# Kernel tuning notes

Measured on AMD Instinct MI355X. Metric: run time of the kernel, lower is better.

The kernel has to match this reference:

```python
import jax, jax.numpy as jnp
import numpy as np

B, T, N, F_IN = 8, 288, 2000, 1
E, ID, H, K = 128, 16, 128, 20
FL = T // 2 + 1  # rfft length = in_len//2 + 1
EPS_NORM = 1e-12
EPS_LN = 1e-8


def setup_inputs() -> dict:
    key = jax.random.key(0)
    k0, k1, k2, k3, k4 = jax.random.split(key, 5)
    return {
        "x": jax.random.normal(k0, (B, T, N, F_IN), jnp.float32),
        "Ex": jax.random.normal(k1, (FL, E), jnp.float32),
        "nodes": jax.random.normal(k2, (N, ID), jnp.float32),
        "Wd": jax.random.normal(k3, (N, E + ID, H), jnp.float32),
        "Wxabs": jax.random.normal(k4, (H, H), jnp.float32),
    }


def reference(x, Ex, nodes, Wd, Wxabs):
    # [B,T,N,F] -> take feature 0 -> [B,N,T]
    xt = jnp.transpose(x[:, :, :, 0], (0, 2, 1))
    xf = jnp.abs(jnp.fft.rfft(xt, axis=-1))  # [B,N,FL]
    # F.normalize p=2 over dim=1 (nodes), then dim=2 (freq): x / max(||x||, eps)
    xf = xf / jnp.clip(jnp.sqrt(jnp.sum(xf * xf, axis=1, keepdims=True)), EPS_NORM)
    xf = xf / jnp.clip(jnp.sqrt(jnp.sum(xf * xf, axis=2, keepdims=True)), EPS_NORM)
    xe = jnp.matmul(xf, Ex)  # [B,N,E]
    # cat(): append static node identity embedding per batch element
    xk = jnp.concatenate(
        [xe, jnp.broadcast_to(nodes, (xe.shape[0], N, ID))], axis=-1
    )  # [B,N,E+ID]
    # per-node weight bmm: [N,B,E+ID] @ [N,E+ID,H] -> [B,N,H]
    x1 = jax.nn.relu(jnp.einsum('bnd,ndh->bnh', xk, Wd))
    # LayerNorm over last two dims [N,H], eps=1e-8, no affine
    mu = jnp.mean(x1, axis=(1, 2), keepdims=True)
    var = jnp.mean((x1 - mu) ** 2, axis=(1, 2), keepdims=True)
    x2 = (x1 - mu) / jnp.sqrt(var + EPS_LN)
    # dropout is identity at inference
    adp = jnp.einsum('bnh,hk->bnk', x2, Wxabs)  # convt
    adj = jnp.einsum('bnh,bmh->bnm', adp, x1)  # [B,N,N]
    adp = jax.nn.relu(adj)
    # dy_mask_graph: per-row topk over dim=2 (torch dim=1 of the [N,N] slice),
    # binary mask via scatter of ones, then elementwise mask
    _, idx = jax.lax.top_k(adp, K)  # [B,N,K]
    bi = jnp.arange(adp.shape[0])[:, None, None]
    ni = jnp.arange(N)[None, :, None]
    mask = jnp.zeros_like(adp).at[bi, ni, idx].set(1.0)
    adj_masked = adp * mask
    return jax.nn.softmax(adj_masked, axis=2)
```

## Files before the change

### kernel.cpp

```cpp
#include <hip/hip_runtime.h>
#include <math.h>

#define BB 8
#define TT 288
#define NN 2000
#define FLEN 145
#define EE 128
#define IDD 16
#define HH 128
#define DKK 144
#define KTOP 20

typedef _Float16 half8 __attribute__((ext_vector_type(8)));
typedef float f32x4 __attribute__((ext_vector_type(4)));
typedef unsigned short ushort_t;

#define OFF_TW  ((size_t)0)
#define SZ_TW   ((size_t)TT*FLEN*2)
#define OFF_XF  (OFF_TW + SZ_TW)
#define SZ_XF   ((size_t)BB*FLEN*NN)
#define OFF_ICN (OFF_XF + SZ_XF)
#define OFF_IRN (OFF_ICN + (size_t)BB*FLEN)
#define OFF_XE  (OFF_IRN + (size_t)BB*NN)
#define SZ_BNH  ((size_t)BB*NN*HH)
#define OFF_X1  (OFF_XE + SZ_BNH)
#define OFF_ADP (OFF_X1 + SZ_BNH)
#define OFF_CSW (OFF_ADP + SZ_BNH)
#define OFF_LNS (OFF_CSW + HH)
#define OFF_LNF (OFF_LNS + 16)

__device__ __forceinline__ float wredSum(float v) {
#pragma unroll
  for (int o = 32; o > 0; o >>= 1) v += __shfl_down(v, o, 64);
  return v;
}
__device__ __forceinline__ float wredMax(float v) {
#pragma unroll
  for (int o = 32; o > 0; o >>= 1) v = fmaxf(v, __shfl_down(v, o, 64));
  return v;
}
__device__ __forceinline__ float wredSumAll(float v) {
#pragma unroll
  for (int o = 32; o > 0; o >>= 1) v += __shfl_xor(v, o, 64);
  return v;
}
__device__ __forceinline__ float wredMaxAll(float v) {
#pragma unroll
  for (int o = 32; o > 0; o >>= 1) v = fmaxf(v, __shfl_xor(v, o, 64));
  return v;
}

__device__ __forceinline__ void split16(float v, ushort_t& hi, ushort_t& lo) {
  _Float16 h = (_Float16)v;
  _Float16 l = (_Float16)(v - (float)h);
  union { _Float16 f; ushort_t u; } a, b;
  a.f = h; b.f = l;
  hi = a.u; lo = b.u;
}

__global__ void k_init(const float* __restrict__ Wx, float* __restrict__ csw,
                       float* __restrict__ lns) {
  int k = threadIdx.x;
  float s = 0.f;
  for (int h = 0; h < HH; ++h) s += Wx[h * HH + k];
  csw[k] = s;
  if (k < 16) lns[k] = 0.f;
}

__global__ void k_tw(float* __restrict__ tw) {
  int id = blockIdx.x * 256 + threadIdx.x;
  if (id >= TT * FLEN) return;
  int t = id / FLEN, f = id % FLEN;
  int r = (t * f) % TT;
  double th = -2.0 * 3.14159265358979323846 * (double)r / (double)TT;
  tw[2 * id]     = (float)cos(th);
  tw[2 * id + 1] = (float)sin(th);
}

__global__ void k_dft(const float* __restrict__ x, const float* __restrict__ tw,
                      float* __restrict__ xf) {
  __shared__ __align__(16) float Xs[16][128];
  __shared__ __align__(16) float TWs[16][32][2];
  const int b = blockIdx.z;
  const int f0 = blockIdx.y * 32;
  const int n0 = blockIdx.x * 128;
  const int tid = threadIdx.x;
  const int tn = tid & 31;
  const int tf = tid >> 5;
  float ar[4][4] = {}, ai[4][4] = {};
  for (int t0 = 0; t0 < TT; t0 += 16) {
    __syncthreads();
    for (int l = tid; l < 512; l += 256) {
      int row = l >> 5, q = l & 31;
      int n = n0 + q * 4;
      const float* src = x + ((size_t)b * TT + (t0 + row)) * NN + n;
      float4 v = make_float4(0, 0, 0, 0);
      if (n + 3 < NN) v = *(const float4*)src;
      else {
        if (n + 0 < NN) v.x = src[0];
        if (n + 1 < NN) v.y = src[1];
        if (n + 2 < NN) v.z = src[2];
        if (n + 3 < NN) v.w = src[3];
      }
      *(float4*)&Xs[row][q * 4] = v;
    }
    for (int l = tid; l < 512; l += 256) {
      int row = l >> 5, ff = l & 31;
      int f = f0 + ff;
      float2 cs = make_float2(0, 0);
      if (f < FLEN) cs = *(const float2*)&tw[((size_t)(t0 + row) * FLEN + f) * 2];
      *(float2*)&TWs[row][ff][0] = cs;
    }
    __syncthreads();
#pragma unroll 4
    for (int t = 0; t < 16; ++t) {
      float4 xv = *(float4*)&Xs[t][tn * 4];
      float xx[4] = {xv.x, xv.y, xv.z, xv.w};
      float4 p0 = *(float4*)&TWs[t][tf * 4][0];
      float4 p1 = *(float4*)&TWs[t][tf * 4 + 2][0];
      float c[4] = {p0.x, p0.z, p1.x, p1.z};
      float s[4] = {p0.y, p0.w, p1.y, p1.w};
#pragma unroll
      for (int i = 0; i < 4; ++i)
#pragma unroll
        for (int j = 0; j < 4; ++j) {
          ar[i][j] = fmaf(xx[j], c[i], ar[i][j]);
          ai[i][j] = fmaf(xx[j], s[i], ai[i][j]);
        }
    }
  }
#pragma unroll
  for (int i = 0; i < 4; ++i) {
    int f = f0 + tf * 4 + i;
    if (f >= FLEN) continue;
    float* dst = &xf[((size_t)b * FLEN + f) * NN];
    float o[4];
#pragma unroll
    for (int j = 0; j < 4; ++j)
      o[j] = sqrtf(ar[i][j] * ar[i][j] + ai[i][j] * ai[i][j]);
    int n = n0 + tn * 4;
    if (n + 3 < NN) *(float4*)&dst[n] = make_float4(o[0], o[1], o[2], o[3]);
    else {
#pragma unroll
      for (int j = 0; j < 4; ++j) if (n + j < NN) dst[n + j] = o[j];
    }
  }
}

__global__ void k_colnorm(const float* __restrict__ xf, float* __restrict__ icn) {
  __shared__ float sc[4];
  int bf = blockIdx.x;
  const float* rowp = xf + (size_t)bf * NN;
  float s = 0.f;
  for (int i = threadIdx.x; i < NN; i += 256) { float v = rowp[i]; s = fmaf(v, v, s); }
  s = wredSum(s);
  int lane = threadIdx.x & 63, w = threadIdx.x >> 6;
  if (lane == 0) sc[w] = s;
  __syncthreads();
  if (threadIdx.x == 0)
    icn[bf] = 1.f / fmaxf(sqrtf(sc[0] + sc[1] + sc[2] + sc[3]), 1e-12f);
}

__global__ void k_rownorm(const float* __restrict__ xf, const float* __restrict__ icn,
                          float* __restrict__ irn) {
  int b = blockIdx.y;
  int n = blockIdx.x * 256 + threadIdx.x;
  if (n >= NN) return;
  float s = 0.f;
  for (int f = 0; f < FLEN; ++f) {
    float v = xf[((size_t)b * FLEN + f) * NN + n] * icn[b * FLEN + f];
    s = fmaf(v, v, s);
  }
  irn[b * NN + n] = 1.f / fmaxf(sqrtf(s), 1e-12f);
}

__global__ void k_xe(const float* __restrict__ xf, const float* __restrict__ icn,
                     const float* __restrict__ irn, const float* __restrict__ Ex,
                     float* __restrict__ xe) {
  __shared__ __align__(16) float As[16][64];
  __shared__ __align__(16) float Bs[16][128];
  const int b = blockIdx.y;
  const int n0 = blockIdx.x * 64;
  const int tid = threadIdx.x;
  const int tn = tid >> 4, te = tid & 15;
  float acc[4][8] = {};
  for (int f0 = 0; f0 < 160; f0 += 16) {
    __syncthreads();
    {
      int kt = tid >> 4, q = tid & 15;
      int f = f0 + kt;
      int n = n0 + q * 4;
      float4 v = make_float4(0, 0, 0, 0);
      if (f < FLEN) {
        float ic = icn[b * FLEN + f];
        const float* src = &xf[((size_t)b * FLEN + f) * NN + n];
        if (n + 3 < NN) v = *(const float4*)src;
        else {
          if (n + 0 < NN) v.x = src[0];
          if (n + 1 < NN) v.y = src[1];
          if (n + 2 < NN) v.z = src[2];
          if (n + 3 < NN) v.w = src[3];
        }
        v.x *= ic; v.y *= ic; v.z *= ic; v.w *= ic;
      }
      *(float4*)&As[kt][q * 4] = v;
    }
    for (int l = tid; l < 512; l += 256) {
      int kt = l >> 5, q = l & 31;
      int f = f0 + kt;
      float4 v = make_float4(0, 0, 0, 0);
      if (f < FLEN) v = *(const float4*)&Ex[(size_t)f * EE + q * 4];
      *(float4*)&Bs[kt][q * 4] = v;
    }
    __syncthreads();
#pragma unroll
    for (int k = 0; k < 16; ++k) {
      float4 a  = *(float4*)&As[k][tn * 4];
      float4 b0 = *(float4*)&Bs[k][te * 4];
      float4 b1 = *(float4*)&Bs[k][64 + te * 4];
      float av[4] = {a.x, a.y, a.z, a.w};
      float bv[8] = {b0.x, b0.y, b0.z, b0.w, b1.x, b1.y, b1.z, b1.w};
#pragma unroll
      for (int i = 0; i < 4; ++i)
#pragma unroll
        for (int j = 0; j < 8; ++j)
          acc[i][j] = fmaf(av[i], bv[j], acc[i][j]);
    }
  }
#pragma unroll
  for (int i = 0; i < 4; ++i) {
    int n = n0 + tn * 4 + i;
    if (n >= NN) continue;
    float sc = irn[b * NN + n];
    float* dst = &xe[((size_t)b * NN + n) * EE];
    *(float4*)&dst[te * 4] =
        make_float4(acc[i][0] * sc, acc[i][1] * sc, acc[i][2] * sc, acc[i][3] * sc);
    *(float4*)&dst[64 + te * 4] =
        make_float4(acc[i][4] * sc, acc[i][5] * sc, acc[i][6] * sc, acc[i][7] * sc);
  }
}

__global__ void k_x1(const float* xe, const float* __restrict__ nodes,
                     const float* __restrict__ Wd, float* __restrict__ x1,
                     ushort_t* x1hl) {
  __shared__ __align__(16) float xk[8][DKK];
  __shared__ float red[4][32][33];
  const int n = blockIdx.x;
  const int tid = threadIdx.x;
  {
    int b = tid >> 5, q = tid & 31;
    *(float4*)&xk[b][q * 4] = *(const float4*)&xe[((size_t)b * NN + n) * EE + q * 4];
  }
  if (tid < 128) {
    int b = tid >> 4, i = tid & 15;
    xk[b][EE + i] = nodes[(size_t)n * IDD + i];
  }
  __syncthreads();
  const int h4 = tid & 31;
  const int dg = tid >> 5;
  float acc[8][4] = {};
  for (int d = dg; d < DKK; d += 8) {
    float4 wv = *(const float4*)&Wd[((size_t)n * DKK + d) * HH + h4 * 4];
#pragma unroll
    for (int b = 0; b < 8; ++b) {
      float xv = xk[b][d];
      acc[b][0] = fmaf(xv, wv.x, acc[b][0]);
      acc[b][1] = fmaf(xv, wv.y, acc[b][1]);
      acc[b][2] = fmaf(xv, wv.z, acc[b][2]);
      acc[b][3] = fmaf(xv, wv.w, acc[b][3]);
    }
  }
#pragma unroll
  for (int b = 0; b < 8; ++b)
#pragma unroll
    for (int j = 0; j < 4; ++j)
      acc[b][j] += __shfl_xor(acc[b][j], 32, 64);
  const int wv_ = tid >> 6, lane = tid & 63;
  if (lane < 32) {
#pragma unroll
    for (int b = 0; b < 8; ++b)
#pragma unroll
      for (int j = 0; j < 4; ++j)
        red[wv_][lane][b * 4 + j] = acc[b][j];
  }
  __syncthreads();
#pragma unroll
  for (int o = 0; o < 4; ++o) {
    int idx = tid + o * 256;
    int b = idx >> 7, h = idx & 127;
    float s = red[0][h >> 2][b * 4 + (h & 3)] + red[1][h >> 2][b * 4 + (h & 3)] +
              red[2][h >> 2][b * 4 + (h & 3)] + red[3][h >> 2][b * 4 + (h & 3)];
    s = fmaxf(s, 0.f);
    x1[((size_t)b * NN + n) * HH + h] = s;
    ushort_t hi, lo;
    split16(s, hi, lo);
    size_t base = ((size_t)b * NN + n) * 256;
    x1hl[base + h] = hi;
    x1hl[base + 128 + h] = lo;
  }
}

__global__ void k_ln_stats(const float* __restrict__ x1, float* __restrict__ lns) {
  __shared__ float sc[4], sc2[4];
  int b = blockIdx.y, chunk = blockIdx.x;
  const float* base = x1 + (size_t)b * NN * HH + (size_t)chunk * 8000;
  float s = 0.f, s2 = 0.f;
  for (int i = threadIdx.x; i < 8000; i += 256) {
    float v = base[i];
    s += v; s2 = fmaf(v, v, s2);
  }
  s = wredSum(s); s2 = wredSum(s2);
  int lane = threadIdx.x & 63, w = threadIdx.x >> 6;
  if (lane == 0) { sc[w] = s; sc2[w] = s2; }
  __syncthreads();
  if (threadIdx.x == 0) {
    atomicAdd(&lns[b], sc[0] + sc[1] + sc[2] + sc[3]);
    atomicAdd(&lns[8 + b], sc2[0] + sc2[1] + sc2[2] + sc2[3]);
  }
}

__global__ void k_ln_final(const float* __restrict__ lns, float* __restrict__ lnf) {
  int b = threadIdx.x;
  if (b < 8) {
    float cnt = (float)(NN * HH);
    float mu = lns[b] / cnt;
    float var = fmaxf(lns[8 + b] / cnt - mu * mu, 0.f);
    lnf[b] = mu;
    lnf[8 + b] = 1.f / sqrtf(var + 1e-8f);
  }
}

__global__ void k_adp(const float* __restrict__ x1, const float* __restrict__ Wx,
                      const float* __restrict__ csw, const float* __restrict__ lnf,
                      ushort_t* __restrict__ adphl) {
  __shared__ __align__(16) float As[16][64];
  __shared__ __align__(16) float Bs[16][128];
  const int r0 = blockIdx.x * 64;
  const int tid = threadIdx.x;
  const int tn = tid >> 4, te = tid & 15;
  float acc[4][8] = {};
  for (int k0 = 0; k0 < HH; k0 += 16) {
    __syncthreads();
    {
      int rr = tid >> 2, kq = tid & 3;
      float4 v = *(const float4*)&x1[(size_t)(r0 + rr) * HH + k0 + kq * 4];
      As[kq * 4 + 0][rr] = v.x;
      As[kq * 4 + 1][rr] = v.y;
      As[kq * 4 + 2][rr] = v.z;
      As[kq * 4 + 3][rr] = v.w;
    }
    for (int l = tid; l < 512; l += 256) {
      int kt = l >> 5, q = l & 31;
      *(float4*)&Bs[kt][q * 4] = *(const float4*)&Wx[(size_t)(k0 + kt) * HH + q * 4];
    }
    __syncthreads();
#pragma unroll
    for (int k = 0; k < 16; ++k) {
      float4 a  = *(float4*)&As[k][tn * 4];
      float4 b0 = *(float4*)&Bs[k][te * 4];
      float4 b1 = *(float4*)&Bs[k][64 + te * 4];
      float av[4] = {a.x, a.y, a.z, a.w};
      float bv[8] = {b0.x, b0.y, b0.z, b0.w, b1.x, b1.y, b1.z, b1.w};
#pragma unroll
      for (int i = 0; i < 4; ++i)
#pragma unroll
        for (int j = 0; j < 8; ++j)
          acc[i][j] = fmaf(av[i], bv[j], acc[i][j]);
    }
  }
  float4 c0 = *(const float4*)&csw[te * 4];
  float4 c1 = *(const float4*)&csw[64 + te * 4];
  float cw[8] = {c0.x, c0.y, c0.z, c0.w, c1.x, c1.y, c1.z, c1.w};
#pragma unroll
  for (int i = 0; i < 4; ++i) {
    int r = r0 + tn * 4 + i;
    int b = r / NN;
    float mu = lnf[b], isd = lnf[8 + b];
    size_t base = (size_t)r * 256;
    ushort_t hi[8], lo[8];
#pragma unroll
    for (int j = 0; j < 8; ++j) {
      float o = (acc[i][j] - mu * cw[j]) * isd;
      split16(o, hi[j], lo[j]);
    }
    ushort4 u;
    u.x = hi[0]; u.y = hi[1]; u.z = hi[2]; u.w = hi[3];
    *(ushort4*)&adphl[base + te * 4] = u;
    u.x = hi[4]; u.y = hi[5]; u.z = hi[6]; u.w = hi[7];
    *(ushort4*)&adphl[base + 64 + te * 4] = u;
    u.x = lo[0]; u.y = lo[1]; u.z = lo[2]; u.w = lo[3];
    *(ushort4*)&adphl[base + 128 + te * 4] = u;
    u.x = lo[4]; u.y = lo[5]; u.z = lo[6]; u.w = lo[7];
    *(ushort4*)&adphl[base + 128 + 64 + te * 4] = u;
  }
}

__global__ __launch_bounds__(256, 2) void k_adjT(
    const ushort_t* __restrict__ adphl, const ushort_t* __restrict__ x1hl,
    float* __restrict__ out) {
  const int b = blockIdx.z;
  const int n0 = blockIdx.y * 16;
  const int tid = threadIdx.x;
  const int w = tid >> 6;
  const int lane = tid & 63;
  const int quad = lane >> 4, r16 = lane & 15;

  half8 Ah[4], Al[4];
  {
    const ushort_t* abase =
        adphl + ((size_t)(b * NN + n0 + r16)) * 256 + quad * 8;
#pragma unroll
    for (int ks = 0; ks < 4; ++ks) {
      Ah[ks] = *(const half8*)(abase + ks * 32);
      Al[ks] = *(const half8*)(abase + 128 + ks * 32);
    }
  }
  const int mbase = blockIdx.x * 512 + w * 128;
  float* obase = out + ((size_t)(b * NN + n0 + quad * 4)) * NN;

  half8 Bh0[4], Bl0[4], Bh1[4], Bl1[4];

#define LOADB(I, BH, BL)                                                      \
  {                                                                           \
    int mt_ = mbase + (I) * 16 + r16;                                         \
    int mc_ = (mt_ < NN) ? mt_ : NN - 1;                                      \
    const ushort_t* bb_ = x1hl + ((size_t)(b * NN + mc_)) * 256 + quad * 8;   \
    BH[0] = *(const half8*)(bb_);       BL[0] = *(const half8*)(bb_ + 128);   \
    BH[1] = *(const half8*)(bb_ + 32);  BL[1] = *(const half8*)(bb_ + 160);   \
    BH[2] = *(const half8*)(bb_ + 64);  BL[2] = *(const half8*)(bb_ + 192);   \
    BH[3] = *(const half8*)(bb_ + 96);  BL[3] = *(const half8*)(bb_ + 224);   \
  }

#define STEP(I, BH, BL, BH2, BL2)                                             \
  {                                                                           \
    if ((I) < 7) LOADB((I) + 1, BH2, BL2);                                    \
    f32x4 acc = (f32x4){0.f, 0.f, 0.f, 0.f};                                  \
    _Pragma("unroll")                                                         \
    for (int ks = 0; ks < 4; ++ks) {                                          \
      acc = __builtin_amdgcn_mfma_f32_16x16x32_f16(Ah[ks], BH[ks], acc, 0, 0, 0); \
      acc = __builtin_amdgcn_mfma_f32_16x16x32_f16(Ah[ks], BL[ks], acc, 0, 0, 0); \
      acc = __builtin_amdgcn_mfma_f32_16x16x32_f16(Al[ks], BH[ks], acc, 0, 0, 0); \
    }                                                                         \
    int mt_ = mbase + (I) * 16 + r16;                                         \
    if (mt_ < NN) {                                                           \
      _Pragma("unroll")                                                       \
      for (int reg = 0; reg < 4; ++reg)                                       \
        obase[(size_t)reg * NN + mt_] = fmaxf(acc[reg], 0.f);                 \
    }                                                                         \
  }

  LOADB(0, Bh0, Bl0);
  STEP(0, Bh0, Bl0, Bh1, Bl1);
  STEP(1, Bh1, Bl1, Bh0, Bl0);
  STEP(2, Bh0, Bl0, Bh1, Bl1);
  STEP(3, Bh1, Bl1, Bh0, Bl0);
  STEP(4, Bh0, Bl0, Bh1, Bl1);
  STEP(5, Bh1, Bl1, Bh0, Bl0);
  STEP(6, Bh0, Bl0, Bh1, Bl1);
  STEP(7, Bh1, Bl1, Bh0, Bl0);
#undef STEP
#undef LOADB
}

__global__ __launch_bounds__(256, 4) void k_topsm(float* out) {
  __shared__ float scrV[4][64];
  __shared__ int scrI[4][64];
  const int tid = threadIdx.x;
  const int w = tid >> 6, lane = tid & 63;
  const int r = blockIdx.x * 4 + w;
  float* g = out + (size_t)r * NN;

  f32x4 V[8];
#pragma unroll
  for (int j = 0; j < 8; ++j) {
    int m0 = j * 256 + lane * 4;
    if (m0 < NN) V[j] = *(const f32x4*)&g[m0];
    else V[j] = (f32x4){-1.f, -1.f, -1.f, -1.f};
  }

  float mx = -1.f, cp = 0.f;
#pragma unroll
  for (int j = 0; j < 8; ++j)
#pragma unroll
    for (int e = 0; e < 4; ++e) {
      mx = fmaxf(mx, V[j][e]);
      cp += (V[j][e] > 0.f) ? 1.f : 0.f;
    }
  const float m = wredMaxAll(mx);
  const float cpos = wredSumAll(cp);
  const float em = expf(-m);

  if (cpos <= 20.5f) {
    float s = 0.f;
#pragma unroll
    for (int j = 0; j < 8; ++j)
#pragma unroll
      for (int e = 0; e < 4; ++e)
        if (V[j][e] > 0.f) s += expf(V[j][e] - m);
    s = wredSumAll(s);
    const float invD = 1.f / (s + (2000.f - cpos) * em);
    const float defv = em * invD;
#pragma unroll
    for (int j = 0; j < 8; ++j) {
      int m0 = j * 256 + lane * 4;
      if (m0 >= NN) continue;
      float4 o;
      o.x = (V[j][0] > 0.f) ? expf(V[j][0] - m) * invD : defv;
      o.y = (V[j][1] > 0.f) ? expf(V[j][1] - m) * invD : defv;
      o.z = (V[j][2] > 0.f) ? expf(V[j][2] - m) * invD : defv;
      o.w = (V[j][3] > 0.f) ? expf(V[j][3] - m) * invD : defv;
      *(float4*)&g[m0] = o;
    }
  } else {
    float tval = 0.f, cf = cpos;
    if (cpos > 64.5f) {
      float tlo = 0.f, thi = m;
      bool found = false;
      for (int it = 0; it < 64 && !found; ++it) {
        float mid = (it < 12)
            ? 0.5f * (tlo + thi)
            : __uint_as_float((__float_as_uint(tlo) + __float_as_uint(thi)) >> 1);
        float c = 0.f;
#pragma unroll
        for (int j = 0; j < 8; ++j)
#pragma unroll
          for (int e = 0; e < 4; ++e)
            c += (V[j][e] > mid) ? 1.f : 0.f;
        c = wredSumAll(c);
        if (c > 64.5f) tlo = mid;
        else if (c < 19.5f) thi = mid;
        else { tval = mid; cf = c; found = true; }
      }
      if (!found) { tval = tlo; cf = 64.f; }
    }
    int cI = (int)(cf + 0.5f);
    if (cI > 64) cI = 64;

    float* sv = scrV[w];
    int* si = scrI[w];
    int base = 0;
#pragma unroll
    for (int j = 0; j < 8; ++j)
#pragma unroll
      for (int e = 0; e < 4; ++e) {
        bool p = V[j][e] > tval;
        unsigned long long msk = __ballot(p);
        if (p) {
          int pos = base + (int)__popcll(msk & ((1ull << lane) - 1ull));
          if (pos < 64) { sv[pos] = V[j][e]; si[pos] = j * 256 + lane * 4 + e; }
        }
        base += (int)__popcll(msk);
      }
    asm volatile("s_waitcnt lgkmcnt(0)" ::: "memory");

    float cv = (lane < cI) ? sv[lane] : -1.f;
    int ci = (lane < cI) ? si[lane] : 0x7fffffff;
#pragma unroll
    for (int k = 2; k <= 64; k <<= 1)
#pragma unroll
      for (int j = k >> 1; j > 0; j >>= 1) {
        float ov = __shfl_xor(cv, j, 64);
        int oi = __shfl_xor(ci, j, 64);
        bool otherBetter = (ov > cv) || (ov == cv && oi < ci);
        bool iAmLow = (lane & j) == 0;
        bool desc = (lane & k) == 0;
        bool take = (desc == iAmLow) ? otherBetter : !otherBetter;
        if (take) { cv = ov; ci = oi; }
      }
    const float t20 = __shfl(cv, 19, 64);
    float e20 = (lane < 20) ? expf(cv - m) : 0.f;
    const float s20 = wredSumAll(e20);
    const float invD = 1.f / (s20 + (2000.f - 20.f) * em);
    const float defv = em * invD;
#pragma unroll
    for (int j = 0; j < 8; ++j) {
      int m0 = j * 256 + lane * 4;
      if (m0 >= NN) continue;
      float4 o;
      o.x = (V[j][0] >= t20) ? expf(V[j][0] - m) * invD : defv;
      o.y = (V[j][1] >= t20) ? expf(V[j][1] - m) * invD : defv;
      o.z = (V[j][2] >= t20) ? expf(V[j][2] - m) * invD : defv;
      o.w = (V[j][3] >= t20) ? expf(V[j][3] - m) * invD : defv;
      *(float4*)&g[m0] = o;
    }
  }
}

extern "C" void kernel_launch(void* const* d_in, const int* in_sizes, int n_in,
                              void* d_out, int out_size, void* d_ws, size_t ws_size,
                              hipStream_t stream) {
  const float* x     = (const float*)d_in[0];
  const float* Ex    = (const float*)d_in[1];
  const float* nodes = (const float*)d_in[2];
  const float* Wd    = (const float*)d_in[3];
  const float* Wx    = (const float*)d_in[4];
  float* out = (float*)d_out;
  float* w = (float*)d_ws;
  float* tw  = w + OFF_TW;
  float* xf  = w + OFF_XF;
  float* icn = w + OFF_ICN;
  float* irn = w + OFF_IRN;
  float* xe  = w + OFF_XE;
  float* x1  = w + OFF_X1;
  float* csw = w + OFF_CSW;
  float* lns = w + OFF_LNS;
  float* lnf = w + OFF_LNF;
  ushort_t* adphl = (ushort_t*)(w + OFF_ADP);
  ushort_t* x1hl  = (ushort_t*)(w + OFF_XE);

  k_init<<<1, 128, 0, stream>>>(Wx, csw, lns);
  k_tw<<<(TT * FLEN + 255) / 256, 256, 0, stream>>>(tw);
  k_dft<<<dim3(16, 5, BB), 256, 0, stream>>>(x, tw, xf);
  k_colnorm<<<BB * FLEN, 256, 0, stream>>>(xf, icn);
  k_rownorm<<<dim3(8, BB), 256, 0, stream>>>(xf, icn, irn);
  k_xe<<<dim3(32, BB), 256, 0, stream>>>(xf, icn, irn, Ex, xe);
  k_x1<<<NN, 256, 0, stream>>>(xe, nodes, Wd, x1, x1hl);
  k_ln_stats<<<dim3(32, BB), 256, 0, stream>>>(x1, lns);
  k_ln_final<<<1, 64, 0, stream>>>(lns, lnf);
  k_adp<<<250, 256, 0, stream>>>(x1, Wx, csw, lnf, adphl);
  k_adjT<<<dim3(4, 125, BB), 256, 0, stream>>>(adphl, x1hl, out);
  k_topsm<<<(BB * NN) / 4, 256, 0, stream>>>(out);
}
```

Measured before the change: 571.2 us.

## Store split-fp16 x1 and adp in MFMA-tiled layout for coalesced fragment loads

The hi/lo fp16 copies of x1 and adp are written in a 16-row tiled layout, where each 16-node tile holds contiguous 8-element fragments ordered by k-slice and quad. The adjacency MFMA kernel can then load each half8 fragment with lane-contiguous addresses instead of 512-byte row strides. The producer kernels now do scattered 2-byte and 8-byte writes into the new layout. A sched_barrier is also added after the B prefetch, which constrains how the compiler interleaves loads with the MFMAs.

```diff
diff --git a/kernel.cpp b/kernel.cpp
--- a/kernel.cpp
+++ b/kernel.cpp
@@ -28,6 +28,7 @@
 #define OFF_CSW (OFF_ADP + SZ_BNH)
 #define OFF_LNS (OFF_CSW + HH)
 #define OFF_LNF (OFF_LNS + 16)
+
 
 __device__ __forceinline__ float wredSum(float v) {
 #pragma unroll
@@ -284,6 +285,7 @@
         red[wv_][lane][b * 4 + j] = acc[b][j];
   }
   __syncthreads();
+  const size_t tbase = (size_t)(n >> 4) * 4096 + (size_t)(n & 15) * 8;
 #pragma unroll
   for (int o = 0; o < 4; ++o) {
     int idx = tid + o * 256;
@@ -294,9 +296,10 @@
     x1[((size_t)b * NN + n) * HH + h] = s;
     ushort_t hi, lo;
     split16(s, hi, lo);
-    size_t base = ((size_t)b * NN + n) * 256;
-    x1hl[base + h] = hi;
-    x1hl[base + 128 + h] = lo;
+    size_t slot = (size_t)b * (125 * 4096) + tbase +
+                  (size_t)((h >> 5) * 512 + ((h >> 3) & 3) * 128 + (h & 7));
+    x1hl[slot] = hi;
+    x1hl[slot + 2048] = lo;
   }
 }
 
@@ -371,27 +374,31 @@
   float4 c0 = *(const float4*)&csw[te * 4];
   float4 c1 = *(const float4*)&csw[64 + te * 4];
   float cw[8] = {c0.x, c0.y, c0.z, c0.w, c1.x, c1.y, c1.z, c1.w};
+  const int c0k = te * 4, c1k = 64 + te * 4;
+  const size_t o0r = (size_t)((c0k >> 5) * 512 + ((c0k >> 3) & 3) * 128 + (c0k & 7));
+  const size_t o1r = (size_t)((c1k >> 5) * 512 + ((c1k >> 3) & 3) * 128 + (c1k & 7));
 #pragma unroll
   for (int i = 0; i < 4; ++i) {
     int r = r0 + tn * 4 + i;
-    int b = r / NN;
+    int b = r / NN, n = r % NN;
     float mu = lnf[b], isd = lnf[8 + b];
-    size_t base = (size_t)r * 256;
     ushort_t hi[8], lo[8];
 #pragma unroll
     for (int j = 0; j < 8; ++j) {
       float o = (acc[i][j] - mu * cw[j]) * isd;
       split16(o, hi[j], lo[j]);
     }
+    size_t slot = (size_t)b * (125 * 4096) + (size_t)(n >> 4) * 4096 +
+                  (size_t)(n & 15) * 8;
     ushort4 u;
     u.x = hi[0]; u.y = hi[1]; u.z = hi[2]; u.w = hi[3];
-    *(ushort4*)&adphl[base + te * 4] = u;
+    *(ushort4*)&adphl[slot + o0r] = u;
     u.x = hi[4]; u.y = hi[5]; u.z = hi[6]; u.w = hi[7];
-    *(ushort4*)&adphl[base + 64 + te * 4] = u;
+    *(ushort4*)&adphl[slot + o1r] = u;
     u.x = lo[0]; u.y = lo[1]; u.z = lo[2]; u.w = lo[3];
-    *(ushort4*)&adphl[base + 128 + te * 4] = u;
+    *(ushort4*)&adphl[slot + 2048 + o0r] = u;
     u.x = lo[4]; u.y = lo[5]; u.z = lo[6]; u.w = lo[7];
-    *(ushort4*)&adphl[base + 128 + 64 + te * 4] = u;
+    *(ushort4*)&adphl[slot + 2048 + o1r] = u;
   }
 }
 
@@ -399,41 +406,44 @@
     const ushort_t* __restrict__ adphl, const ushort_t* __restrict__ x1hl,
     float* __restrict__ out) {
   const int b = blockIdx.z;
-  const int n0 = blockIdx.y * 16;
+  const int tA = blockIdx.y;
+  const int n0 = tA * 16;
   const int tid = threadIdx.x;
   const int w = tid >> 6;
   const int lane = tid & 63;
   const int quad = lane >> 4, r16 = lane & 15;
+  const int lq = quad * 128 + r16 * 8;
 
   half8 Ah[4], Al[4];
   {
-    const ushort_t* abase =
-        adphl + ((size_t)(b * NN + n0 + r16)) * 256 + quad * 8;
+    const ushort_t* abase = adphl + ((size_t)(b * 125 + tA)) * 4096 + lq;
 #pragma unroll
     for (int ks = 0; ks < 4; ++ks) {
-      Ah[ks] = *(const half8*)(abase + ks * 32);
-      Al[ks] = *(const half8*)(abase + 128 + ks * 32);
+      Ah[ks] = *(const half8*)(abase + ks * 512);
+      Al[ks] = *(const half8*)(abase + 2048 + ks * 512);
     }
   }
   const int mbase = blockIdx.x * 512 + w * 128;
+  const ushort_t* Bb = x1hl + (size_t)b * (125 * 4096) + lq;
   float* obase = out + ((size_t)(b * NN + n0 + quad * 4)) * NN;
 
   half8 Bh0[4], Bl0[4], Bh1[4], Bl1[4];
 
 #define LOADB(I, BH, BL)                                                      \
   {                                                                           \
-    int mt_ = mbase + (I) * 16 + r16;                                         \
-    int mc_ = (mt_ < NN) ? mt_ : NN - 1;                                      \
-    const ushort_t* bb_ = x1hl + ((size_t)(b * NN + mc_)) * 256 + quad * 8;   \
-    BH[0] = *(const half8*)(bb_);       BL[0] = *(const half8*)(bb_ + 128);   \
-    BH[1] = *(const half8*)(bb_ + 32);  BL[1] = *(const half8*)(bb_ + 160);   \
-    BH[2] = *(const half8*)(bb_ + 64);  BL[2] = *(const half8*)(bb_ + 192);   \
-    BH[3] = *(const half8*)(bb_ + 96);  BL[3] = *(const half8*)(bb_ + 224);   \
+    int tB_ = (mbase + (I) * 16) >> 4;                                        \
+    if (tB_ > 124) tB_ = 124;         \
+    const ushort_t* bb_ = Bb + (size_t)tB_ * 4096;                            \
+    BH[0] = *(const half8*)(bb_);        BL[0] = *(const half8*)(bb_ + 2048); \
+    BH[1] = *(const half8*)(bb_ + 512);  BL[1] = *(const half8*)(bb_ + 2560); \
+    BH[2] = *(const half8*)(bb_ + 1024); BL[2] = *(const half8*)(bb_ + 3072); \
+    BH[3] = *(const half8*)(bb_ + 1536); BL[3] = *(const half8*)(bb_ + 3584); \
   }
 
 #define STEP(I, BH, BL, BH2, BL2)                                             \
   {                                                                           \
     if ((I) < 7) LOADB((I) + 1, BH2, BL2);                                    \
+    __builtin_amdgcn_sched_barrier(0);      \
     f32x4 acc = (f32x4){0.f, 0.f, 0.f, 0.f};                                  \
     _Pragma("unroll")                                                         \
     for (int ks = 0; ks < 4; ++ks) {                                          \
```

Result: faster. 490.7 us (-14.1%).
